# Performance work log

Measured on AMD Instinct MI355X. Metric: run time of the kernel, lower is better.

The kernel has to match this reference:

```python
import jax, jax.numpy as jnp
import numpy as np

D_MODEL = 512
NHEAD = 8
HEAD_DIM = D_MODEL // NHEAD
DFF = 2048
KSIZE = 3
EPS = 1e-5


def conv1d(x, w, b, pad):
    # x: [B, Cin, S], w: [Cout, Cin, K] -> [B, Cout, S]
    y = jax.lax.conv_general_dilated(x, w, window_strides=(1,), padding=[(pad, pad)],
                                     dimension_numbers=("NCH", "OIH", "NCH"))
    return y + b[None, :, None]


def layernorm(x, g, b):
    mu = jnp.mean(x, axis=-1, keepdims=True)
    var = jnp.mean(jnp.square(x - mu), axis=-1, keepdims=True)
    return (x - mu) * jax.lax.rsqrt(var + EPS) * g + b


def setup_inputs() -> dict:
    key = jax.random.key(0)
    ks = jax.random.split(key, 16)
    B, S = 8, 1024
    # conv init: normal(0, sqrt(2/(K*out_ch))) per head (out_ch = HEAD_DIM), bias 0.1
    sq = np.sqrt(2.0 / (KSIZE * HEAD_DIM)).astype(np.float32)
    sv = np.sqrt(2.0 / (1 * HEAD_DIM)).astype(np.float32)
    inp = {
        "src": jax.random.normal(ks[0], (B, S, D_MODEL), jnp.float32),
        "Wq": jax.random.normal(ks[1], (D_MODEL, D_MODEL, KSIZE), jnp.float32) * sq,
        "bq": jnp.full((D_MODEL,), 0.1, jnp.float32),
        "Wk": jax.random.normal(ks[2], (D_MODEL, D_MODEL, KSIZE), jnp.float32) * sq,
        "bk": jnp.full((D_MODEL,), 0.1, jnp.float32),
        "Wv": jax.random.normal(ks[3], (D_MODEL, D_MODEL, 1), jnp.float32) * sv,
        "bv": jnp.full((D_MODEL,), 0.1, jnp.float32),
        "Wo": jax.random.normal(ks[4], (D_MODEL, D_MODEL), jnp.float32) * 0.02,
        "bo": jnp.zeros((D_MODEL,), jnp.float32),
        "W1": jax.random.normal(ks[5], (DFF, D_MODEL), jnp.float32) * 0.02,
        "b1": jnp.zeros((DFF,), jnp.float32),
        "W2": jax.random.normal(ks[6], (D_MODEL, DFF), jnp.float32) * 0.02,
        "b2": jnp.zeros((D_MODEL,), jnp.float32),
        "g1": jnp.ones((D_MODEL,), jnp.float32),
        "be1": jnp.zeros((D_MODEL,), jnp.float32),
        "g2": jnp.ones((D_MODEL,), jnp.float32),
        "be2": jnp.zeros((D_MODEL,), jnp.float32),
    }
    return inp


def reference(src, Wq, bq, Wk, bk, Wv, bv, Wo, bo, W1, b1, W2, b2, g1, be1, g2, be2):
    B, S, D = src.shape
    H, hd = NHEAD, HEAD_DIM
    xt = jnp.transpose(src, (0, 2, 1))  # [B, D, S]
    # H per-head convs over the same input == one conv with D output channels
    q = conv1d(xt, Wq, bq, (KSIZE - 1) // 2).reshape(B, H, hd, S)
    k = conv1d(xt, Wk, bk, (KSIZE - 1) // 2).reshape(B, H, hd, S)
    v = conv1d(xt, Wv, bv, 0).reshape(B, H, hd, S)
    # NOTE: source divides by head_dim (not sqrt(head_dim))
    scores = jnp.einsum("bhds,bhdt->bhst", q, k) / hd
    att = jax.nn.softmax(scores, axis=-1)  # [B, H, S, S]
    av = jnp.einsum("bhst,bhdt->bhsd", att, v)  # [B, H, S, hd]
    av = jnp.transpose(av, (0, 2, 1, 3)).reshape(B, S, D)
    sa = av @ Wo.T + bo
    x = layernorm(src + sa, g1, be1)  # post-norm (norm_first=False)
    ff = jax.nn.relu(x @ W1.T + b1) @ W2.T + b2
    return layernorm(x + ff, g2, be2)
```

## Files before the change

kernel.cpp:

```cpp
#include <hip/hip_runtime.h>
#include <hip/hip_bf16.h>

using bf16 = __hip_bfloat16;
typedef __attribute__((ext_vector_type(8))) short s8v;
typedef __attribute__((ext_vector_type(4))) short s4v;
typedef __attribute__((ext_vector_type(4))) float f32x4;

#define DEV __device__ __forceinline__

DEV f32x4 mfma16(s8v a, s8v b, f32x4 c) {
    return __builtin_amdgcn_mfma_f32_16x16x32_bf16(a, b, c, 0, 0, 0);
}

DEV void gl_to_lds16(const bf16* g, bf16* l) {
    __builtin_amdgcn_global_load_lds(
        (const __attribute__((address_space(1))) void*)g,
        (__attribute__((address_space(3))) void*)l, 16, 0, 0);
}

DEV unsigned short bfbits(bf16 h) { union { bf16 h; unsigned short u; } c; c.h = h; return c.u; }
DEV unsigned pk2(float a, float b) {
    return (unsigned)bfbits(__float2bfloat16(a)) | ((unsigned)bfbits(__float2bfloat16(b)) << 16);
}
DEV unsigned pk2t(float a, float b) {
    return (__float_as_uint(a) >> 16) | (__float_as_uint(b) & 0xffff0000u);
}
DEV void unpk8(uint4 u, float* x) {
    const unsigned uu[4] = {u.x, u.y, u.z, u.w};
#pragma unroll
    for (int j = 0; j < 4; j++) {
        x[2 * j]     = __uint_as_float(uu[j] << 16);
        x[2 * j + 1] = __uint_as_float(uu[j] & 0xffff0000u);
    }
}

__global__ __launch_bounds__(256)
void convert_all(const float* __restrict__ src, const float* __restrict__ Wv,
                 const float* __restrict__ Wo, const float* __restrict__ W1,
                 const float* __restrict__ W2, bf16* __restrict__ srcb,
                 bf16* __restrict__ Wvb, bf16* __restrict__ Wob, bf16* __restrict__ W1b,
                 bf16* __restrict__ W2b) {
    const long long i4 = ((long long)blockIdx.x * 256 + threadIdx.x) * 4;
    const float* in;
    bf16* outp;
    long long off;
    if (i4 < 4194304)      { in = src; outp = srcb; off = 0; }
    else if (i4 < 4456448) { in = Wv;  outp = Wvb;  off = 4194304; }
    else if (i4 < 4718592) { in = Wo;  outp = Wob;  off = 4456448; }
    else if (i4 < 5767168) { in = W1;  outp = W1b;  off = 4718592; }
    else                   { in = W2;  outp = W2b;  off = 5767168; }
    const long long j = i4 - off;
    const float4 v = *(const float4*)(in + j);
    uint2 o;
    o.x = pk2(v.x, v.y);
    o.y = pk2(v.z, v.w);
    *(uint2*)(outp + j) = o;
}

__global__ __launch_bounds__(256)
void prep_kernel(const float* __restrict__ Wq, const float* __restrict__ Wk,
                 bf16* __restrict__ WqT, bf16* __restrict__ WkT, bf16* __restrict__ zp) {
    const int i = blockIdx.x * 256 + threadIdx.x;
    if (i < 512) zp[i] = __float2bfloat16(0.f);
    const int dk = i >> 18, rem = i & 262143, co = rem >> 9, ci = rem & 511;
    const size_t s = (size_t)co * 1536 + ci * 3 + dk;
    WqT[i] = __float2bfloat16(Wq[s]);
    WkT[i] = __float2bfloat16(Wk[s]);
}

__global__ __launch_bounds__(256)
void conv_qk(const bf16* __restrict__ src, const bf16* __restrict__ WqT,
             const bf16* __restrict__ WkT, const float* __restrict__ bq,
             const float* __restrict__ bk, bf16* __restrict__ Qo, bf16* __restrict__ Ko,
             const bf16* __restrict__ zp) {
    const int z = blockIdx.z, b = z & 7, isK = z >> 3;
    const bf16* WT = isK ? WkT : WqT;
    const float* bias = isK ? bk : bq;
    bf16* out = isK ? Ko : Qo;
    const float qs = isK ? 1.0f : 0.022542109951390054f;
    const bf16* S = src + ((size_t)b << 19);
    const int m0 = blockIdx.x * 128, n0 = blockIdx.y * 128;
    const int tid = threadIdx.x, w = tid >> 6, l = tid & 63;
    const int wm = (w >> 1) << 6, wn = (w & 1) << 6;
    __shared__ __align__(16) bf16 As[4096], Bs[4096];
    f32x4 acc[4][4] = {};
    for (int k0 = 0; k0 < 1536; k0 += 32) {
        const int dk = k0 >> 9, ci0 = k0 & 511;
        if (k0) __syncthreads();
#pragma unroll
        for (int i = 0; i < 2; i++) {
            const int srow = m0 + i * 64 + w * 16 + (l >> 2) - 1 + dk;
            const bf16* ga = (srow >= 0 && srow < 1024)
                                 ? S + (size_t)srow * 512 + ci0 + (l & 3) * 8
                                 : zp + (l & 3) * 8;
            gl_to_lds16(ga, &As[i * 2048 + w * 512]);
            const int co = n0 + i * 64 + w * 16 + (l >> 2);
            gl_to_lds16(WT + ((size_t)dk << 18) + (size_t)co * 512 + ci0 + (l & 3) * 8,
                        &Bs[i * 2048 + w * 512]);
        }
        __syncthreads();
        s8v af[4], bfv[4];
#pragma unroll
        for (int x = 0; x < 4; x++) {
            af[x]  = *(const s8v*)&As[(wm + x * 16 + (l & 15)) * 32 + ((l >> 4) << 3)];
            bfv[x] = *(const s8v*)&Bs[(wn + x * 16 + (l & 15)) * 32 + ((l >> 4) << 3)];
        }
#pragma unroll
        for (int mt = 0; mt < 4; mt++)
#pragma unroll
            for (int nt = 0; nt < 4; nt++) acc[mt][nt] = mfma16(af[mt], bfv[nt], acc[mt][nt]);
    }
#pragma unroll
    for (int nt = 0; nt < 4; nt++) {
        const int co = n0 + wn + nt * 16 + (l & 15);
        const float bn = bias[co];
        const size_t obase = ((size_t)b << 19) + ((size_t)(co >> 6) << 16) + (co & 63);
#pragma unroll
        for (int mt = 0; mt < 4; mt++)
#pragma unroll
            for (int r = 0; r < 4; r++) {
                const int s = m0 + wm + mt * 16 + ((l >> 4) << 2) + r;
                out[obase + (size_t)s * 64] = __float2bfloat16((acc[mt][nt][r] + bn) * qs);
            }
    }
}

template <int EPI>
__global__ __launch_bounds__(256)
void gemm_nt(const bf16* __restrict__ A, const bf16* __restrict__ B,
             const float* __restrict__ bias, void* __restrict__ C, int M, int N, int K,
             int lda, int ldb, int ldc, long long aOff, long long bOff, long long cOff) {
    const int m0 = blockIdx.x * 128, n0 = blockIdx.y * 128, z = blockIdx.z;
    A += (size_t)z * aOff;
    B += (size_t)z * bOff;
    const int tid = threadIdx.x, w = tid >> 6, l = tid & 63;
    const int wm = (w >> 1) << 6, wn = (w & 1) << 6;
    __shared__ __align__(16) bf16 As[4096], Bs[4096];
    f32x4 acc[4][4] = {};
    for (int k0 = 0; k0 < K; k0 += 32) {
        if (k0) __syncthreads();
#pragma unroll
        for (int i = 0; i < 2; i++) {
            gl_to_lds16(A + (size_t)(m0 + i * 64 + w * 16 + (l >> 2)) * lda + k0 + (l & 3) * 8,
                        &As[i * 2048 + w * 512]);
            gl_to_lds16(B + (size_t)(n0 + i * 64 + w * 16 + (l >> 2)) * ldb + k0 + (l & 3) * 8,
                        &Bs[i * 2048 + w * 512]);
        }
        __syncthreads();
        s8v af[4], bfv[4];
#pragma unroll
        for (int x = 0; x < 4; x++) {
            af[x]  = *(const s8v*)&As[(wm + x * 16 + (l & 15)) * 32 + ((l >> 4) << 3)];
            bfv[x] = *(const s8v*)&Bs[(wn + x * 16 + (l & 15)) * 32 + ((l >> 4) << 3)];
        }
#pragma unroll
        for (int mt = 0; mt < 4; mt++)
#pragma unroll
            for (int nt = 0; nt < 4; nt++) acc[mt][nt] = mfma16(af[mt], bfv[nt], acc[mt][nt]);
    }
#pragma unroll
    for (int nt = 0; nt < 4; nt++) {
        const int n = n0 + wn + nt * 16 + (l & 15);
        const float bn = (EPI == 1) ? bias[n] : 0.f;
#pragma unroll
        for (int mt = 0; mt < 4; mt++)
#pragma unroll
            for (int r = 0; r < 4; r++) {
                const int m = m0 + wm + mt * 16 + ((l >> 4) << 2) + r;
                float v = acc[mt][nt][r];
                const size_t off = (size_t)z * cOff + (size_t)m * ldc + n;
                if (EPI == 3) {
                    ((float*)C)[off] = v;
                } else {
                    v += (EPI == 2) ? bias[m] : bn;
                    if (EPI == 1) v = fmaxf(v, 0.f);
                    ((bf16*)C)[off] = __float2bfloat16(v);
                }
            }
    }
}

__global__ __launch_bounds__(256)
void attn_kernel(const bf16* __restrict__ Q, const bf16* __restrict__ K,
                 const bf16* __restrict__ V, bf16* __restrict__ av) {
    const int bh = blockIdx.x, b = bh >> 3, h = bh & 7;
    const bf16* Qp = Q + ((size_t)bh << 16);
    const bf16* Kp = K + ((size_t)bh << 16);
    const bf16* Vp = V + ((size_t)bh << 16);
    const int tid = threadIdx.x, w = tid >> 6, l = tid & 63;
    const int lq = l & 15, quad = l >> 4;
    const int q0 = blockIdx.y * 128 + w * 16;
    __shared__ __align__(16) bf16 Ks[4096], Vs[4096], Ps[8192];
    bf16* Pw0 = &Ps[(w * 2 + 0) * 1024];
    bf16* Pw1 = &Ps[(w * 2 + 1) * 1024];
    const s8v qf00 = *(const s8v*)&Qp[(size_t)(q0 + lq) * 64 + quad * 8];
    const s8v qf01 = *(const s8v*)&Qp[(size_t)(q0 + lq) * 64 + 32 + quad * 8];
    const s8v qf10 = *(const s8v*)&Qp[(size_t)(q0 + 64 + lq) * 64 + quad * 8];
    const s8v qf11 = *(const s8v*)&Qp[(size_t)(q0 + 64 + lq) * 64 + 32 + quad * 8];
    f32x4 o0[4] = {}, o1[4] = {};
    float l0 = 0.f, l1 = 0.f;
    const int sr = tid >> 3;
    const int scb = tid & 7;
    const int swz_st = (scb ^ (sr & 7)) * 8;
    const int rdz0 = (quad ^ (lq & 7)) * 8;
    const int rdz1 = ((quad + 4) ^ (lq & 7)) * 8;
    const int pwz = ((quad >> 1) ^ (lq & 7)) * 8 + (quad & 1) * 4;
    s8v kA = *(const s8v*)&Kp[(size_t)sr * 64 + scb * 8];
    s8v kB = *(const s8v*)&Kp[(size_t)(sr + 32) * 64 + scb * 8];
    s8v vA = *(const s8v*)&Vp[(size_t)sr * 1024 + scb * 8];
    s8v vB = *(const s8v*)&Vp[(size_t)(sr + 32) * 1024 + scb * 8];
    for (int t0 = 0; t0 < 1024; t0 += 64) {
        __syncthreads();
        *(s8v*)&Ks[sr * 64 + swz_st] = kA;
        *(s8v*)&Ks[(sr + 32) * 64 + swz_st] = kB;
        *(s8v*)&Vs[sr * 64 + swz_st] = vA;
        *(s8v*)&Vs[(sr + 32) * 64 + swz_st] = vB;
        if (t0 + 64 < 1024) {
            const int t1 = t0 + 64;
            kA = *(const s8v*)&Kp[(size_t)(t1 + sr) * 64 + scb * 8];
            kB = *(const s8v*)&Kp[(size_t)(t1 + sr + 32) * 64 + scb * 8];
            vA = *(const s8v*)&Vp[(size_t)sr * 1024 + t1 + scb * 8];
            vB = *(const s8v*)&Vp[(size_t)(sr + 32) * 1024 + t1 + scb * 8];
        }
        __syncthreads();
        f32x4 st0[4] = {}, st1[4] = {};
#pragma unroll
        for (int tt = 0; tt < 4; tt++) {
            const int rb = (tt * 16 + lq) * 64;
            const s8v ka0 = *(const s8v*)&Ks[rb + rdz0];
            const s8v ka1 = *(const s8v*)&Ks[rb + rdz1];
            st0[tt] = mfma16(ka0, qf00, st0[tt]);
            st0[tt] = mfma16(ka1, qf01, st0[tt]);
            st1[tt] = mfma16(ka0, qf10, st1[tt]);
            st1[tt] = mfma16(ka1, qf11, st1[tt]);
        }
        float cs0 = 0.f, cs1 = 0.f;
#pragma unroll
        for (int tt = 0; tt < 4; tt++) {
            const float a0 = __builtin_amdgcn_exp2f(st0[tt][0]);
            const float a1 = __builtin_amdgcn_exp2f(st0[tt][1]);
            const float a2 = __builtin_amdgcn_exp2f(st0[tt][2]);
            const float a3 = __builtin_amdgcn_exp2f(st0[tt][3]);
            cs0 += (a0 + a1) + (a2 + a3);
            uint2 pkv;
            pkv.x = pk2t(a0, a1);
            pkv.y = pk2t(a2, a3);
            *(uint2*)&Pw0[lq * 64 + (pwz ^ (tt * 16))] = pkv;
            const float b0 = __builtin_amdgcn_exp2f(st1[tt][0]);
            const float b1 = __builtin_amdgcn_exp2f(st1[tt][1]);
            const float b2 = __builtin_amdgcn_exp2f(st1[tt][2]);
            const float b3 = __builtin_amdgcn_exp2f(st1[tt][3]);
            cs1 += (b0 + b1) + (b2 + b3);
            uint2 pkw;
            pkw.x = pk2t(b0, b1);
            pkw.y = pk2t(b2, b3);
            *(uint2*)&Pw1[lq * 64 + (pwz ^ (tt * 16))] = pkw;
        }
        cs0 += __shfl_xor(cs0, 16);
        cs0 += __shfl_xor(cs0, 32);
        cs1 += __shfl_xor(cs1, 16);
        cs1 += __shfl_xor(cs1, 32);
        l0 += cs0;
        l1 += cs1;
        const s8v pb00 = *(const s8v*)&Pw0[lq * 64 + rdz0];
        const s8v pb01 = *(const s8v*)&Pw0[lq * 64 + rdz1];
        const s8v pb10 = *(const s8v*)&Pw1[lq * 64 + rdz0];
        const s8v pb11 = *(const s8v*)&Pw1[lq * 64 + rdz1];
#pragma unroll
        for (int dt = 0; dt < 4; dt++) {
            const int rb = (dt * 16 + lq) * 64;
            const s8v va0 = *(const s8v*)&Vs[rb + rdz0];
            const s8v va1 = *(const s8v*)&Vs[rb + rdz1];
            o0[dt] = mfma16(va0, pb00, o0[dt]);
            o0[dt] = mfma16(va1, pb01, o0[dt]);
            o1[dt] = mfma16(va0, pb10, o1[dt]);
            o1[dt] = mfma16(va1, pb11, o1[dt]);
        }
    }
    const float i0 = 1.f / l0, i1 = 1.f / l1;
    const size_t rb0 = ((size_t)b * 1024 + q0 + lq) * 512 + h * 64;
    const size_t rb1 = rb0 + (size_t)64 * 512;
#pragma unroll
    for (int dt = 0; dt < 4; dt++) {
        uint2 ov;
        ov.x = pk2(o0[dt][0] * i0, o0[dt][1] * i0);
        ov.y = pk2(o0[dt][2] * i0, o0[dt][3] * i0);
        *(uint2*)&av[rb0 + dt * 16 + quad * 4] = ov;
        uint2 ow;
        ow.x = pk2(o1[dt][0] * i1, o1[dt][1] * i1);
        ow.y = pk2(o1[dt][2] * i1, o1[dt][3] * i1);
        *(uint2*)&av[rb1 + dt * 16 + quad * 4] = ow;
    }
}

template <int MODE>
__global__ __launch_bounds__(256)
void ln_kernel(const void* __restrict__ A, const float* __restrict__ P0,
               const float* __restrict__ P1, const float* __restrict__ bias,
               const float* __restrict__ g, const float* __restrict__ be,
               void* __restrict__ outp) {
    const int w = threadIdx.x >> 6, l = threadIdx.x & 63;
    const size_t row = (size_t)blockIdx.x * 4 + w;
    const size_t base = row * 512 + l * 8;
    float x[8];
    if (MODE == 1) {
        const float4 a0 = *(const float4*)((const float*)A + base);
        const float4 a1 = *(const float4*)((const float*)A + base + 4);
        x[0] = a0.x; x[1] = a0.y; x[2] = a0.z; x[3] = a0.w;
        x[4] = a1.x; x[5] = a1.y; x[6] = a1.z; x[7] = a1.w;
    } else {
        unpk8(*(const uint4*)((const bf16*)A + base), x);
    }
    const float4 p00 = *(const float4*)(P0 + base);
    const float4 p01 = *(const float4*)(P0 + base + 4);
    const float4 p10 = *(const float4*)(P1 + base);
    const float4 p11 = *(const float4*)(P1 + base + 4);
    const float4 bb0 = *(const float4*)(bias + l * 8);
    const float4 bb1 = *(const float4*)(bias + l * 8 + 4);
    x[0] += p00.x + p10.x + bb0.x; x[1] += p00.y + p10.y + bb0.y;
    x[2] += p00.z + p10.z + bb0.z; x[3] += p00.w + p10.w + bb0.w;
    x[4] += p01.x + p11.x + bb1.x; x[5] += p01.y + p11.y + bb1.y;
    x[6] += p01.z + p11.z + bb1.z; x[7] += p01.w + p11.w + bb1.w;
    float s = 0.f, sq = 0.f;
#pragma unroll
    for (int j = 0; j < 8; j++) { s += x[j]; sq += x[j] * x[j]; }
#pragma unroll
    for (int off = 1; off < 64; off <<= 1) {
        s += __shfl_xor(s, off);
        sq += __shfl_xor(sq, off);
    }
    const float mean = s * (1.f / 512.f);
    const float var = sq * (1.f / 512.f) - mean * mean;
    const float rstd = rsqrtf(fmaxf(var, 0.f) + 1e-5f);
    const float4 g0 = *(const float4*)(g + l * 8);
    const float4 g1 = *(const float4*)(g + l * 8 + 4);
    const float4 e0 = *(const float4*)(be + l * 8);
    const float4 e1 = *(const float4*)(be + l * 8 + 4);
    const float gv[8] = {g0.x, g0.y, g0.z, g0.w, g1.x, g1.y, g1.z, g1.w};
    const float ev[8] = {e0.x, e0.y, e0.z, e0.w, e1.x, e1.y, e1.z, e1.w};
    float y[8];
#pragma unroll
    for (int j = 0; j < 8; j++) y[j] = (x[j] - mean) * rstd * gv[j] + ev[j];
    if (MODE == 1) {
        uint4 o;
        o.x = pk2(y[0], y[1]); o.y = pk2(y[2], y[3]);
        o.z = pk2(y[4], y[5]); o.w = pk2(y[6], y[7]);
        *(uint4*)((bf16*)outp + base) = o;
    } else {
        *(float4*)((float*)outp + base)     = make_float4(y[0], y[1], y[2], y[3]);
        *(float4*)((float*)outp + base + 4) = make_float4(y[4], y[5], y[6], y[7]);
    }
}

extern "C" void kernel_launch(void* const* d_in, const int* in_sizes, int n_in, void* d_out,
                              int out_size, void* d_ws, size_t ws_size, hipStream_t stream) {
    const float* src = (const float*)d_in[0];
    const float* Wq = (const float*)d_in[1];
    const float* bq = (const float*)d_in[2];
    const float* Wk = (const float*)d_in[3];
    const float* bk = (const float*)d_in[4];
    const float* Wv = (const float*)d_in[5];
    const float* bv = (const float*)d_in[6];
    const float* Wo = (const float*)d_in[7];
    const float* bo = (const float*)d_in[8];
    const float* W1 = (const float*)d_in[9];
    const float* b1 = (const float*)d_in[10];
    const float* W2 = (const float*)d_in[11];
    const float* b2 = (const float*)d_in[12];
    const float* g1 = (const float*)d_in[13];
    const float* be1 = (const float*)d_in[14];
    const float* g2 = (const float*)d_in[15];
    const float* be2 = (const float*)d_in[16];
    float* out = (float*)d_out;

    char* base = (char*)d_ws;
    bf16* srcb = (bf16*)(base + 0);
    bf16* Qb   = (bf16*)(base + 8388608);
    bf16* Kb   = (bf16*)(base + 16777216);
    bf16* Vb   = (bf16*)(base + 25165824);
    bf16* ff1  = (bf16*)(base + 0);
    bf16* avb  = (bf16*)(base + 33554432);
    bf16* xb   = avb;
    float* saf = (float*)(base + 41943040);
    bf16* WqT  = (bf16*)(base + 75497472);
    bf16* WkT  = (bf16*)(base + 77070336);
    bf16* zp   = (bf16*)(base + 78643200);
    bf16* Wvb  = (bf16*)(base + 78644224);
    bf16* Wob  = (bf16*)(base + 79168512);
    bf16* W1b  = (bf16*)(base + 79692800);
    bf16* W2b  = (bf16*)(base + 81789952);

    convert_all<<<6656, 256, 0, stream>>>(src, Wv, Wo, W1, W2, srcb, Wvb, Wob, W1b, W2b);
    prep_kernel<<<3072, 256, 0, stream>>>(Wq, Wk, WqT, WkT, zp);
    conv_qk<<<dim3(8, 4, 16), 256, 0, stream>>>(srcb, WqT, WkT, bq, bk, Qb, Kb, zp);
    gemm_nt<2><<<dim3(4, 8, 8), 256, 0, stream>>>(Wvb, srcb, bv, Vb, 512, 1024, 512,
                                                  512, 512, 1024, 0, 524288, 524288);
    attn_kernel<<<dim3(64, 8), 256, 0, stream>>>(Qb, Kb, Vb, avb);
    gemm_nt<3><<<dim3(64, 4, 2), 256, 0, stream>>>(avb, Wob, nullptr, saf, 8192, 512, 256,
                                                   512, 512, 512, 256, 256, 4194304LL);
    ln_kernel<1><<<2048, 256, 0, stream>>>(src, saf, saf + 4194304, bo, g1, be1, xb);
    gemm_nt<1><<<dim3(64, 16, 1), 256, 0, stream>>>(xb, W1b, b1, ff1, 8192, 2048, 512,
                                                    512, 512, 2048, 0, 0, 0);
    gemm_nt<3><<<dim3(64, 4, 2), 256, 0, stream>>>(ff1, W2b, nullptr, saf, 8192, 512, 1024,
                                                   2048, 2048, 512, 1024, 1024, 4194304LL);
    ln_kernel<2><<<2048, 256, 0, stream>>>(xb, saf, saf + 4194304, b2, g2, be2, out);
}
```

Measured before the change: 276.5 us.

## Reuse one source tile across three conv taps and merge prep kernels

The Q/K conv GEMM now loads a single 130-row source tile per 32-channel step and reads it at three row offsets, one per kernel tap. Before, each tap reloaded its own shifted source tile. Weight tiles for all three taps are staged together, which cuts source global loads and barrier count and triples the MFMA work per synchronisation, at the cost of more LDS (about 33KB). The two preprocessing kernels are also folded into one launch to save a kernel launch.

```diff
diff --git a/kernel.cpp b/kernel.cpp
--- a/kernel.cpp
+++ b/kernel.cpp
@@ -35,37 +35,38 @@
 }
 
 __global__ __launch_bounds__(256)
-void convert_all(const float* __restrict__ src, const float* __restrict__ Wv,
-                 const float* __restrict__ Wo, const float* __restrict__ W1,
-                 const float* __restrict__ W2, bf16* __restrict__ srcb,
-                 bf16* __restrict__ Wvb, bf16* __restrict__ Wob, bf16* __restrict__ W1b,
-                 bf16* __restrict__ W2b) {
-    const long long i4 = ((long long)blockIdx.x * 256 + threadIdx.x) * 4;
-    const float* in;
-    bf16* outp;
-    long long off;
-    if (i4 < 4194304)      { in = src; outp = srcb; off = 0; }
-    else if (i4 < 4456448) { in = Wv;  outp = Wvb;  off = 4194304; }
-    else if (i4 < 4718592) { in = Wo;  outp = Wob;  off = 4456448; }
-    else if (i4 < 5767168) { in = W1;  outp = W1b;  off = 4718592; }
-    else                   { in = W2;  outp = W2b;  off = 5767168; }
-    const long long j = i4 - off;
-    const float4 v = *(const float4*)(in + j);
-    uint2 o;
-    o.x = pk2(v.x, v.y);
-    o.y = pk2(v.z, v.w);
-    *(uint2*)(outp + j) = o;
-}
-
-__global__ __launch_bounds__(256)
-void prep_kernel(const float* __restrict__ Wq, const float* __restrict__ Wk,
-                 bf16* __restrict__ WqT, bf16* __restrict__ WkT, bf16* __restrict__ zp) {
-    const int i = blockIdx.x * 256 + threadIdx.x;
-    if (i < 512) zp[i] = __float2bfloat16(0.f);
-    const int dk = i >> 18, rem = i & 262143, co = rem >> 9, ci = rem & 511;
-    const size_t s = (size_t)co * 1536 + ci * 3 + dk;
-    WqT[i] = __float2bfloat16(Wq[s]);
-    WkT[i] = __float2bfloat16(Wk[s]);
+void prep_all(const float* __restrict__ src, const float* __restrict__ Wv,
+              const float* __restrict__ Wo, const float* __restrict__ W1,
+              const float* __restrict__ W2, const float* __restrict__ Wq,
+              const float* __restrict__ Wk, bf16* __restrict__ srcb,
+              bf16* __restrict__ Wvb, bf16* __restrict__ Wob, bf16* __restrict__ W1b,
+              bf16* __restrict__ W2b, bf16* __restrict__ WqT, bf16* __restrict__ WkT,
+              bf16* __restrict__ zp) {
+    const int bid = blockIdx.x;
+    if (bid < 6656) {
+        const long long i4 = ((long long)bid * 256 + threadIdx.x) * 4;
+        const float* in;
+        bf16* outp;
+        long long off;
+        if (i4 < 4194304)      { in = src; outp = srcb; off = 0; }
+        else if (i4 < 4456448) { in = Wv;  outp = Wvb;  off = 4194304; }
+        else if (i4 < 4718592) { in = Wo;  outp = Wob;  off = 4456448; }
+        else if (i4 < 5767168) { in = W1;  outp = W1b;  off = 4718592; }
+        else                   { in = W2;  outp = W2b;  off = 5767168; }
+        const long long j = i4 - off;
+        const float4 v = *(const float4*)(in + j);
+        uint2 o;
+        o.x = pk2(v.x, v.y);
+        o.y = pk2(v.z, v.w);
+        *(uint2*)(outp + j) = o;
+    } else {
+        const int i = (bid - 6656) * 256 + threadIdx.x;
+        if (i < 512) zp[i] = __float2bfloat16(0.f);
+        const int dk = i >> 18, rem = i & 262143, co = rem >> 9, ci = rem & 511;
+        const size_t s = (size_t)co * 1536 + ci * 3 + dk;
+        WqT[i] = __float2bfloat16(Wq[s]);
+        WkT[i] = __float2bfloat16(Wk[s]);
+    }
 }
 
 __global__ __launch_bounds__(256)
@@ -81,45 +82,61 @@
     const bf16* S = src + ((size_t)b << 19);
     const int m0 = blockIdx.x * 128, n0 = blockIdx.y * 128;
     const int tid = threadIdx.x, w = tid >> 6, l = tid & 63;
+    const int lq = l & 15, quad = l >> 4;
     const int wm = (w >> 1) << 6, wn = (w & 1) << 6;
-    __shared__ __align__(16) bf16 As[4096], Bs[4096];
+    __shared__ __align__(16) bf16 As[4224], Bs[12288];
     f32x4 acc[4][4] = {};
-    for (int k0 = 0; k0 < 1536; k0 += 32) {
-        const int dk = k0 >> 9, ci0 = k0 & 511;
-        if (k0) __syncthreads();
-#pragma unroll
-        for (int i = 0; i < 2; i++) {
-            const int srow = m0 + i * 64 + w * 16 + (l >> 2) - 1 + dk;
+    for (int ci0 = 0; ci0 < 512; ci0 += 32) {
+        if (ci0) __syncthreads();
+#pragma unroll
+        for (int j = 0; j < 2; j++) {
+            const int r = j * 64 + w * 16 + (l >> 2);
+            const int srow = m0 - 1 + r;
             const bf16* ga = (srow >= 0 && srow < 1024)
                                  ? S + (size_t)srow * 512 + ci0 + (l & 3) * 8
                                  : zp + (l & 3) * 8;
-            gl_to_lds16(ga, &As[i * 2048 + w * 512]);
-            const int co = n0 + i * 64 + w * 16 + (l >> 2);
-            gl_to_lds16(WT + ((size_t)dk << 18) + (size_t)co * 512 + ci0 + (l & 3) * 8,
-                        &Bs[i * 2048 + w * 512]);
-        }
+            gl_to_lds16(ga, &As[(j * 64 + w * 16) * 32]);
+        }
+        if (tid < 8) {
+            const int srow = m0 + 127 + (l >> 2);
+            const bf16* ga = (srow < 1024) ? S + (size_t)srow * 512 + ci0 + (l & 3) * 8
+                                           : zp + (l & 3) * 8;
+            gl_to_lds16(ga, &As[128 * 32]);
+        }
+#pragma unroll
+        for (int dk = 0; dk < 3; dk++)
+#pragma unroll
+            for (int j = 0; j < 2; j++) {
+                const int co = n0 + j * 64 + w * 16 + (l >> 2);
+                gl_to_lds16(WT + ((size_t)dk << 18) + (size_t)co * 512 + ci0 + (l & 3) * 8,
+                            &Bs[dk * 4096 + (j * 64 + w * 16) * 32]);
+            }
         __syncthreads();
-        s8v af[4], bfv[4];
-#pragma unroll
-        for (int x = 0; x < 4; x++) {
-            af[x]  = *(const s8v*)&As[(wm + x * 16 + (l & 15)) * 32 + ((l >> 4) << 3)];
-            bfv[x] = *(const s8v*)&Bs[(wn + x * 16 + (l & 15)) * 32 + ((l >> 4) << 3)];
-        }
-#pragma unroll
-        for (int mt = 0; mt < 4; mt++)
-#pragma unroll
-            for (int nt = 0; nt < 4; nt++) acc[mt][nt] = mfma16(af[mt], bfv[nt], acc[mt][nt]);
+#pragma unroll
+        for (int dk = 0; dk < 3; dk++) {
+            s8v af[4], bfv[4];
+#pragma unroll
+            for (int x = 0; x < 4; x++) {
+                af[x]  = *(const s8v*)&As[(wm + x * 16 + lq + dk) * 32 + quad * 8];
+                bfv[x] = *(const s8v*)&Bs[dk * 4096 + (wn + x * 16 + lq) * 32 + quad * 8];
+            }
+#pragma unroll
+            for (int mt = 0; mt < 4; mt++)
+#pragma unroll
+                for (int nt = 0; nt < 4; nt++)
+                    acc[mt][nt] = mfma16(af[mt], bfv[nt], acc[mt][nt]);
+        }
     }
 #pragma unroll
     for (int nt = 0; nt < 4; nt++) {
-        const int co = n0 + wn + nt * 16 + (l & 15);
+        const int co = n0 + wn + nt * 16 + lq;
         const float bn = bias[co];
         const size_t obase = ((size_t)b << 19) + ((size_t)(co >> 6) << 16) + (co & 63);
 #pragma unroll
         for (int mt = 0; mt < 4; mt++)
 #pragma unroll
             for (int r = 0; r < 4; r++) {
-                const int s = m0 + wm + mt * 16 + ((l >> 4) << 2) + r;
+                const int s = m0 + wm + mt * 16 + quad * 4 + r;
                 out[obase + (size_t)s * 64] = __float2bfloat16((acc[mt][nt][r] + bn) * qs);
             }
     }
@@ -390,8 +407,8 @@
     bf16* W1b  = (bf16*)(base + 79692800);
     bf16* W2b  = (bf16*)(base + 81789952);
 
-    convert_all<<<6656, 256, 0, stream>>>(src, Wv, Wo, W1, W2, srcb, Wvb, Wob, W1b, W2b);
-    prep_kernel<<<3072, 256, 0, stream>>>(Wq, Wk, WqT, WkT, zp);
+    prep_all<<<9728, 256, 0, stream>>>(src, Wv, Wo, W1, W2, Wq, Wk, srcb, Wvb, Wob, W1b,
+                                       W2b, WqT, WkT, zp);
     conv_qk<<<dim3(8, 4, 16), 256, 0, stream>>>(srcb, WqT, WkT, bq, bk, Qb, Kb, zp);
     gemm_nt<2><<<dim3(4, 8, 8), 256, 0, stream>>>(Wvb, srcb, bv, Vb, 512, 1024, 512,
                                                   512, 512, 1024, 0, 524288, 524288);
```

New measurement: 267.5 us. 3.2% less time.
